# Performance work log

Measured on AMD Instinct MI355X. Metric: run time of the kernel, lower is better.

The kernel has to match this reference:

```python
import jax, jax.numpy as jnp
import numpy as np

B, T, R, A = 4, 40, 2000, 36864
H = W = 64
C = 256
PP = 7
RED = 16.0
NCLS = 21
NPOS = 64   # rois_per_image*B//4
NNEG = 192  # rois_per_image*B*3//4
DH = 1024

def _iou(b1, b2):
    # boxes are (top,left,bottom,right)
    t = jnp.maximum(b1[..., 0], b2[..., 0])
    l = jnp.maximum(b1[..., 1], b2[..., 1])
    b = jnp.minimum(b1[..., 2], b2[..., 2])
    r = jnp.minimum(b1[..., 3], b2[..., 3])
    inter = jnp.clip(b - t, 0.0) * jnp.clip(r - l, 0.0)
    a1 = (b1[..., 2] - b1[..., 0]) * (b1[..., 3] - b1[..., 1])
    a2 = (b2[..., 2] - b2[..., 0]) * (b2[..., 3] - b2[..., 1])
    return inter / (a1 + a2 - inter)

def _smooth_l1(p, t):
    d = jnp.abs(p - t)
    return jnp.mean(jnp.where(d < 1.0, 0.5 * d * d, d - 0.5))

def _roi_pool(fm, rois):
    # fm [B,C,H,W], rois [N,5] = (img_id, top,left,bottom,right) in feature-map coords
    fmt = jnp.transpose(fm, (0, 2, 3, 1))  # [B,H,W,C]
    n = rois[:, 0].astype(jnp.int32)[:, None, None]
    t, l, b, r = rois[:, 1], rois[:, 2], rois[:, 3], rois[:, 4]
    g = (jnp.arange(PP, dtype=fm.dtype) + 0.5) / PP
    ys = jnp.clip(t[:, None] + g * (b - t)[:, None], 0.0, H - 1.0)
    xs = jnp.clip(l[:, None] + g * (r - l)[:, None], 0.0, W - 1.0)
    y0 = jnp.floor(ys).astype(jnp.int32)
    x0 = jnp.floor(xs).astype(jnp.int32)
    y1 = jnp.minimum(y0 + 1, H - 1)
    x1 = jnp.minimum(x0 + 1, W - 1)
    wy = (ys - y0)[:, :, None, None]
    wx = (xs - x0)[:, None, :, None]
    def gat(yi, xi):
        return fmt[n, yi[:, :, None], xi[:, None, :], :]  # [N,PP,PP,C]
    v = (gat(y0, x0) * (1 - wy) * (1 - wx) + gat(y0, x1) * (1 - wy) * wx
         + gat(y1, x0) * wy * (1 - wx) + gat(y1, x1) * wy * wx)
    return v.reshape(v.shape[0], -1)  # [N, PP*PP*C]

def _forward(nms_reg, nms_cls, feature_maps, bboxes, classes, anchors, rpn_reg, rpn_cls, W1, b1, Wr, br, Wc, bc):
    # ---------------- RPN trainer: anchor/target matching ----------------
    iou_a = _iou(bboxes[:, :, None, :], anchors[None, None, :, :])   # [B,T,A]
    max_iou = jnp.max(iou_a, axis=1)                                  # [B,A]
    tidx = jnp.argmax(iou_a, axis=1)
    max_tgt = jnp.take_along_axis(bboxes, jnp.broadcast_to(tidx[:, :, None], (B, A, 4)), axis=1)
    mask = (max_iou > 0.5).reshape(-1)
    pos = jnp.nonzero(mask, size=128)[0]        # first 128 positives, flat order (matches cls[mask][:128])
    neg = jnp.nonzero(~mask, size=256 - B)[0]   # torch quirk: 256 - len(mask_matched) = 256 - B
    clsf = rpn_cls.reshape(-1)
    logits = jnp.concatenate([clsf[pos], clsf[neg]])
    lbl = jnp.concatenate([jnp.ones(128, dtype=logits.dtype), jnp.zeros(256 - B, dtype=logits.dtype)])
    rpn_cls_loss = jnp.mean(jnp.maximum(logits, 0) - logits * lbl + jnp.log1p(jnp.exp(-jnp.abs(logits))))
    anc_f = jnp.broadcast_to(anchors[None], (B, A, 4)).reshape(-1, 4)
    rpn_reg_loss = _smooth_l1(rpn_reg.reshape(-1, 4)[pos], max_tgt.reshape(-1, 4)[pos] - anc_f[pos]) / 4.0

    # ------------- RCNN trainer: proposal matching + sampling -------------
    iou_r = _iou(nms_reg[:, None, :, :], bboxes[:, :, None, :])  # [B,T,R]
    iou_m = jnp.max(iou_r, axis=1)                               # [B,R]
    ridx = jnp.argmax(iou_r, axis=1)
    iou_f = iou_m.reshape(-1)
    posr = jnp.nonzero(iou_f > 0.5, size=NPOS)[0]                # first NPOS positives, flat order
    negscore = jnp.where(iou_f <= 0.5, iou_f, -jnp.inf)
    negr = jax.lax.top_k(negscore, NNEG)[1]                      # negatives sorted by IoU descending
    cls_g = jnp.take_along_axis(classes, ridx, axis=1).reshape(-1)
    cls_s = jnp.concatenate([cls_g[posr], jnp.zeros(NNEG, dtype=cls_g.dtype)])
    imid = jnp.repeat(jnp.arange(B, dtype=nms_reg.dtype), R)
    nmsf = nms_reg.reshape(-1, 4)
    sel = jnp.concatenate([posr, negr])
    rois = jnp.concatenate([imid[sel][:, None], nmsf[sel]], axis=1)  # [256,5]
    feat = _roi_pool(feature_maps, rois)
    hmid = jax.nn.relu(feat @ W1 + b1)
    rreg = hmid @ Wr + br
    rcls = hmid @ Wc + bc
    logp = jax.nn.log_softmax(rcls, axis=-1)
    rcnn_cls_loss = -jnp.mean(jnp.take_along_axis(logp, cls_s[:, None], axis=1))
    posb = nmsf[posr]
    rounded = jnp.concatenate([jnp.floor(posb[:, :2] * RED), jnp.ceil(posb[:, 2:] * RED)], axis=1) / RED
    mb = jnp.take_along_axis(bboxes, jnp.broadcast_to(ridx[:, :, None], (B, R, 4)), axis=1).reshape(-1, 4)[posr]
    tgt = mb - rounded
    pr = rreg[:NPOS]
    rcnn_reg_loss = sum(_smooth_l1(pr[:, c], tgt[:, c]) for c in range(4)) / 4.0
    offset = sum(jnp.mean(jnp.abs(pr[:, c] - tgt[:, c])) for c in range(4)) / 4.0
    acc = jnp.mean((jnp.argmax(rcls[:NPOS], axis=-1) == cls_s[:NPOS]).astype(jnp.float32))
    return rpn_cls_loss, rpn_reg_loss, rcnn_cls_loss, rcnn_reg_loss, acc, offset

def _boxes(k, shape):
    k1, k2 = jax.random.split(k)
    c = jax.random.uniform(k1, shape + (2,), minval=10.0, maxval=54.0)
    h = jax.random.uniform(k2, shape + (2,), minval=3.0, maxval=8.0)
    return jnp.concatenate([c - h, c + h], axis=-1)  # (top,left,bottom,right)

def setup_inputs():
    key = jax.random.key(0)
    ks = jax.random.split(key, 13)
    base = _boxes(ks[0], (T,))
    shift = jax.random.uniform(ks[1], (B, T, 2), minval=-0.2, maxval=0.2)
    bboxes = base[None] + jnp.concatenate([shift, shift], axis=-1)  # guarantees >=128 RPN positives
    classes = jax.random.randint(ks[2], (B, T), 1, NCLS)
    anchors = _boxes(ks[3], (A,)).at[:T].set(base)
    nms_reg = _boxes(ks[4], (B, R))
    shift2 = jax.random.uniform(ks[5], (B, T, 2), minval=-0.1, maxval=0.1)
    nms_reg = nms_reg.at[:, :T].set(bboxes + jnp.concatenate([shift2, shift2], axis=-1))  # >=64 RCNN positives
    nms_cls = jax.random.normal(ks[6], (B, R))
    feature_maps = jax.random.normal(ks[7], (B, C, H, W))
    rpn_reg = 0.1 * jax.random.normal(ks[8], (B, A, 4))
    rpn_cls = jax.random.normal(ks[9], (B, A))
    D = PP * PP * C
    W1 = jax.random.normal(ks[10], (D, DH)) * float(1.0 / np.sqrt(D))
    b1 = jnp.zeros((DH,))
    Wr = jax.random.normal(ks[11], (DH, 4)) * float(1.0 / np.sqrt(DH))
    br = jnp.zeros((4,))
    Wc = jax.random.normal(ks[12], (DH, NCLS)) * float(1.0 / np.sqrt(DH))
    bc = jnp.zeros((NCLS,))
    return dict(nms_reg=nms_reg, nms_cls=nms_cls, feature_maps=feature_maps, bboxes=bboxes,
                classes=classes, anchors=anchors, rpn_reg=rpn_reg, rpn_cls=rpn_cls,
                W1=W1, b1=b1, Wr=Wr, br=br, Wc=Wc, bc=bc)

def reference(nms_reg, nms_cls, feature_maps, bboxes, classes, anchors, rpn_reg, rpn_cls, W1, b1, Wr, br, Wc, bc):
    return _forward(nms_reg, nms_cls, feature_maps, bboxes, classes, anchors, rpn_reg, rpn_cls, W1, b1, Wr, br, Wc, bc)
```

## Files before the change

### kernel.cpp

```cpp
#include <hip/hip_runtime.h>

typedef unsigned short u16;
typedef unsigned long long u64;

constexpr int cB = 4, cT = 40, cR = 2000, cA = 36864;
constexpr int cH = 64, cW = 64, cC = 256, cPP = 7;
constexpr int cNCLS = 21, cNPOS = 64, cNNEG = 192, cDH = 1024;
constexpr int cD = cPP * cPP * cC;
constexpr int cBA = cB * cA;
constexpr int cBR = cB * cR;
constexpr int NW64 = cBA / 64;
constexpr int SPLITS = 14;
constexpr int KCH = cD / SPLITS;
constexpr int BK = 64;
constexpr int NITER = KCH / BK;
constexpr unsigned POSKEY = 0x007FFFFFu;

constexpr size_t O_TIDX  = 0;
constexpr size_t O_MASKW = 589824;
constexpr size_t O_KEYS  = 608256;
constexpr size_t O_RIDXG = 640256;
constexpr size_t O_SEL   = 672256;
constexpr size_t O_CLS   = 673280;
constexpr size_t O_ROIS  = 674304;
constexpr size_t O_TGT   = 678400;
constexpr size_t O_FMT   = 1048576;
constexpr size_t O_FEAT  = O_FMT + 8388608;
constexpr size_t O_CPART = O_FEAT + 6422528;

__device__ __forceinline__ float b2f(u16 u) {
  return __uint_as_float(((unsigned)u) << 16);
}
__device__ __forceinline__ u16 f2b(float f) {
  unsigned x = __float_as_uint(f);
  unsigned r = x + 0x7FFFu + ((x >> 16) & 1u);
  return (u16)(r >> 16);
}
__device__ __forceinline__ unsigned f2key(float f) {
  unsigned b = __float_as_uint(f);
  return b ^ ((b & 0x80000000u) ? 0xFFFFFFFFu : 0x80000000u);
}

typedef __attribute__((ext_vector_type(8))) short short8;
typedef __attribute__((ext_vector_type(4))) float f32x4;

__global__ __launch_bounds__(256) void k_front(
    const float* __restrict__ bboxes, const float* __restrict__ anchors,
    const float* __restrict__ nms_reg, const float* __restrict__ fm,
    int* __restrict__ tidx, u64* __restrict__ maskw,
    unsigned* __restrict__ keys, int* __restrict__ ridxg,
    u16* __restrict__ fmt) {
  __shared__ float sfm[64 * 65];
  int bid = blockIdx.x;
  if (bid < 576) {
    float* sb = sfm;
    int b = bid / 144;
    if (threadIdx.x < cT * 4) sb[threadIdx.x] = bboxes[b * cT * 4 + threadIdx.x];
    __syncthreads();
    int i = bid * 256 + threadIdx.x;
    int a = i - b * cA;
    float4 av = ((const float4*)anchors)[a];
    float at = av.x, al = av.y, ab = av.z, ar = av.w;
    float area_a = (ab - at) * (ar - al);
    float best = -1.0f; int bi = 0;
    for (int t = 0; t < cT; ++t) {
      float bt = sb[t * 4], bl = sb[t * 4 + 1], bbv = sb[t * 4 + 2], brv = sb[t * 4 + 3];
      float ih = fmaxf(fminf(bbv, ab) - fmaxf(bt, at), 0.0f);
      float iw = fmaxf(fminf(brv, ar) - fmaxf(bl, al), 0.0f);
      float inter = ih * iw;
      float a1 = (bbv - bt) * (brv - bl);
      float iou = inter / (a1 + area_a - inter);
      if (iou > best) { best = iou; bi = t; }
    }
    tidx[i] = bi;
    u64 bal = __ballot(best > 0.5f);
    if ((threadIdx.x & 63) == 0) maskw[i >> 6] = bal;
  } else if (bid < 608) {
    float* sb = sfm;
    for (int j = threadIdx.x; j < cB * cT * 4; j += 256) sb[j] = bboxes[j];
    __syncthreads();
    int i = (bid - 576) * 256 + threadIdx.x;
    if (i >= cBR) return;
    int b = i / cR;
    float4 nv = ((const float4*)nms_reg)[i];
    float nt = nv.x, nl = nv.y, nb = nv.z, nr = nv.w;
    float area_n = (nb - nt) * (nr - nl);
    float best = -1.0f; int bi = 0;
    for (int t = 0; t < cT; ++t) {
      const float* bx = &sb[(b * cT + t) * 4];
      float ih = fmaxf(fminf(bx[2], nb) - fmaxf(bx[0], nt), 0.0f);
      float iw = fmaxf(fminf(bx[3], nr) - fmaxf(bx[1], nl), 0.0f);
      float inter = ih * iw;
      float a1 = (bx[2] - bx[0]) * (bx[3] - bx[1]);
      float iou = inter / (a1 + area_n - inter);
      if (iou > best) { best = iou; bi = t; }
    }
    keys[i] = (best <= 0.5f) ? f2key(best) : POSKEY;
    ridxg[i] = bi;
  } else {
    int f = bid - 608;
    int b = f >> 8;
    int c0 = ((f >> 6) & 3) * 64;
    int p0 = (f & 63) * 64;
    int t = threadIdx.x;
    int pL = (t & 15) * 4, cL = t >> 4;
    #pragma unroll
    for (int i = 0; i < 4; ++i) {
      int c = cL + i * 16;
      float4 v = *(const float4*)&fm[((size_t)b * cC + c0 + c) * (cH * cW) + p0 + pL];
      sfm[c * 65 + pL] = v.x; sfm[c * 65 + pL + 1] = v.y;
      sfm[c * 65 + pL + 2] = v.z; sfm[c * 65 + pL + 3] = v.w;
    }
    __syncthreads();
    int pW = t >> 2, cg = (t & 3) * 16;
    unsigned pk[8];
    #pragma unroll
    for (int j = 0; j < 8; ++j) {
      unsigned lo = f2b(sfm[(cg + 2 * j) * 65 + pW]);
      unsigned hi = f2b(sfm[(cg + 2 * j + 1) * 65 + pW]);
      pk[j] = lo | (hi << 16);
    }
    u16* dst = &fmt[((size_t)b * (cH * cW) + p0 + pW) * cC + c0 + cg];
    *(uint4*)dst = *(uint4*)&pk[0];
    *(uint4*)(dst + 8) = *(uint4*)&pk[4];
  }
}

__global__ __launch_bounds__(1024) void k_select(
    const u64* __restrict__ maskw, const int* __restrict__ tidx,
    const float* __restrict__ rpn_cls, const float* __restrict__ rpn_reg,
    const float* __restrict__ bboxes, const float* __restrict__ anchors,
    const unsigned* __restrict__ keysg, const int* __restrict__ ridxg,
    const float* __restrict__ nms_reg, const int* __restrict__ classes,
    int* __restrict__ sel, int* __restrict__ cls_s,
    float* __restrict__ rois, float* __restrict__ tgt,
    float* __restrict__ out) {
  __shared__ __align__(16) char smem[50688];
  __shared__ float s_scalF[2];
  __shared__ int s_scalI[3];
  int tid = threadIdx.x, lane = tid & 63, w = tid >> 6;
  u64 lmask = (1ULL << lane) - 1ULL;

  if (blockIdx.x == 0) {
    if (tid < 4) out[2 + tid] = 0.0f;
    u64* s_w   = (u64*)smem;
    int* s_pre = (int*)(smem + 18432);
    int* s_cw  = (int*)(smem + 19008);
    int* s_pos = (int*)(smem + 19584);
    int* s_neg = (int*)(smem + 20096);
    for (int k = tid; k < NW64; k += 1024) s_w[k] = maskw[k];
    if (tid < 128) s_pos[tid] = 0;
    if (tid < 252) s_neg[tid] = 0;
    if (tid == 0) { s_scalF[0] = 0.0f; s_scalF[1] = 0.0f; }
    __syncthreads();
    if (tid < 144) {
      int c = 0;
      #pragma unroll
      for (int k2 = 0; k2 < 16; ++k2) c += __popcll(s_w[tid * 16 + k2]);
      s_cw[tid] = c;
    }
    __syncthreads();
    if (tid == 0) {
      int run = 0;
      for (int ch = 0; ch < 144; ++ch) { s_pre[ch] = run; run += s_cw[ch]; }
    }
    __syncthreads();
    for (int ch = w; ch < 144; ch += 16) {
      int pbase = s_pre[ch];
      int nbase = ch * 1024 - pbase;
      if (pbase >= 128 && nbase >= 252) continue;
      int pc = 0;
      #pragma unroll
      for (int s2 = 0; s2 < 16; ++s2) {
        u64 word = s_w[ch * 16 + s2];
        bool m = (word >> lane) & 1ULL;
        int prefP = __popcll(word & lmask);
        int idx = ch * 1024 + s2 * 64 + lane;
        if (m) {
          int g = pbase + pc + prefP;
          if (g < 128) s_pos[g] = idx;
        } else {
          int g = nbase + (s2 * 64 + lane) - (pc + prefP);
          if (g < 252) s_neg[g] = idx;
        }
        pc += __popcll(word);
      }
    }
    __syncthreads();
    if (tid < 380) {
      int flat; float lbl;
      if (tid < 128) { flat = s_pos[tid]; lbl = 1.0f; }
      else           { flat = s_neg[tid - 128]; lbl = 0.0f; }
      float l = rpn_cls[flat];
      float term = fmaxf(l, 0.0f) - l * lbl + log1pf(expf(-fabsf(l)));
      atomicAdd(&s_scalF[0], term);
    }
    if (tid < 512) {
      int j = tid >> 2, c = tid & 3;
      int flat = s_pos[j];
      int b = flat / cA, a = flat - b * cA;
      int t = tidx[flat];
      float p = rpn_reg[flat * 4 + c];
      float tg = bboxes[(b * cT + t) * 4 + c] - anchors[a * 4 + c];
      float d = fabsf(p - tg);
      float sl = (d < 1.0f) ? 0.5f * d * d : d - 0.5f;
      atomicAdd(&s_scalF[1], sl);
    }
    __syncthreads();
    if (tid == 0) {
      out[0] = s_scalF[0] / 380.0f;
      out[1] = s_scalF[1] / 512.0f / 4.0f;
    }
  } else {
    unsigned* s_key = (unsigned*)smem;
    int* s_hist = (int*)(smem + 32000);
    int* s_pc   = (int*)(smem + 48384);
    int* s_wsum = (int*)(smem + 48896);
    int* s_wsuf = (int*)(smem + 48960);
    int* s_posr = (int*)(smem + 49024);
    int* s_negr = (int*)(smem + 49280);

    for (int i = tid; i < cBR; i += 1024) s_key[i] = keysg[i];
    if (tid < 64) s_posr[tid] = 0;
    __syncthreads();

    {
      int myv = 0; int mypre[8];
      #pragma unroll
      for (int p = 0; p < 8; ++p) {
        int i = p * 1024 + tid;
        bool v = (i < cBR) && (s_key[i] == POSKEY);
        u64 bal = __ballot(v);
        if (lane == 0) s_pc[p * 16 + w] = __popcll(bal);
        mypre[p] = __popcll(bal & lmask);
        myv |= v ? (1 << p) : 0;
      }
      __syncthreads();
      if (tid == 0) {
        int run = 0;
        for (int k = 0; k < 128; ++k) { int t = s_pc[k]; s_pc[k] = run; run += t; }
      }
      __syncthreads();
      #pragma unroll
      for (int p = 0; p < 8; ++p) {
        if (myv & (1 << p)) {
          int g = s_pc[p * 16 + w] + mypre[p];
          if (g < 64) s_posr[g] = p * 1024 + tid;
        }
      }
    }

    unsigned thr = 0; int G = 0;
    int need = cNNEG;
    #pragma unroll
    for (int lvl = 0; lvl < 3; ++lvl) {
      __syncthreads();
      #pragma unroll
      for (int k = 0; k < 4; ++k) s_hist[tid * 4 + k] = 0;
      __syncthreads();
      #pragma unroll
      for (int p = 0; p < 8; ++p) {
        int i = p * 1024 + tid;
        if (i < cBR) {
          unsigned key = s_key[i];
          int bkt = -1;
          if (lvl == 0) bkt = key >> 20;
          else if (lvl == 1) { if ((key >> 20) == (thr >> 20)) bkt = (key >> 8) & 0xFFF; }
          else { if ((key >> 8) == (thr >> 8)) bkt = (key & 0xFF) << 4; }
          if (bkt >= 0) atomicAdd(&s_hist[bkt], 1);
        }
      }
      __syncthreads();
      int local0 = s_hist[tid * 4 + 0], local1 = s_hist[tid * 4 + 1];
      int local2 = s_hist[tid * 4 + 2], local3 = s_hist[tid * 4 + 3];
      int lsum = local0 + local1 + local2 + local3;
      int x = lsum;
      #pragma unroll
      for (int off = 1; off < 64; off <<= 1) {
        int t = __shfl_down(x, off, 64);
        if (lane + off < 64) x += t;
      }
      if (lane == 0) s_wsum[w] = x;
      __syncthreads();
      if (tid == 0) {
        int run = 0;
        for (int wi = 15; wi >= 0; --wi) { s_wsuf[wi] = run; run += s_wsum[wi]; }
      }
      __syncthreads();
      int above = s_wsuf[w] + (x - lsum);
      int run = above;
      int loc[4] = {local3, local2, local1, local0};
      #pragma unroll
      for (int j = 0; j < 4; ++j) {
        int S = run + loc[j];
        if (run < need && S >= need) { s_scalI[0] = tid * 4 + (3 - j); s_scalI[1] = run; }
        run = S;
      }
      __syncthreads();
      int bS = s_scalI[0], ov = s_scalI[1];
      if (lvl == 0) thr = ((unsigned)bS) << 20;
      else if (lvl == 1) thr |= ((unsigned)bS) << 8;
      else thr |= ((unsigned)bS) >> 4;
      G += ov;
      need -= ov;
    }

    if (tid == 0) s_scalI[2] = 0;
    __syncthreads();
    #pragma unroll
    for (int p = 0; p < 8; ++p) {
      int i = p * 1024 + tid;
      if (i < cBR && s_key[i] > thr) {
        int slot = atomicAdd(&s_scalI[2], 1);
        s_negr[slot] = i;
      }
    }
    {
      __syncthreads();
      int myv = 0; int mypre[8];
      #pragma unroll
      for (int p = 0; p < 8; ++p) {
        int i = p * 1024 + tid;
        bool v = (i < cBR) && (s_key[i] == thr);
        u64 bal = __ballot(v);
        if (lane == 0) s_pc[p * 16 + w] = __popcll(bal);
        mypre[p] = __popcll(bal & lmask);
        myv |= v ? (1 << p) : 0;
      }
      __syncthreads();
      if (tid == 0) {
        int run = 0;
        for (int k = 0; k < 128; ++k) { int t = s_pc[k]; s_pc[k] = run; run += t; }
      }
      __syncthreads();
      #pragma unroll
      for (int p = 0; p < 8; ++p) {
        if (myv & (1 << p)) {
          int g = s_pc[p * 16 + w] + mypre[p];
          if (g < need) s_negr[G + g] = p * 1024 + tid;
        }
      }
    }
    __syncthreads();

    if (tid < 256) {
      int flat = (tid < 64) ? s_posr[tid] : s_negr[tid - 64];
      sel[tid] = flat;
      int b = flat / cR;
      #pragma unroll
      for (int c = 0; c < 4; ++c) rois[tid * 4 + c] = nms_reg[flat * 4 + c];
      cls_s[tid] = (tid < 64) ? classes[b * cT + ridxg[flat]] : 0;
      if (tid < 64) {
        int mt = ridxg[flat];
        #pragma unroll
        for (int c = 0; c < 4; ++c) {
          float v = nms_reg[flat * 4 + c];
          float rr = ((c < 2) ? floorf(v * 16.0f) : ceilf(v * 16.0f)) / 16.0f;
          float mbv = bboxes[(b * cT + mt) * 4 + c];
          tgt[tid * 4 + c] = mbv - rr;
        }
      }
    }
  }
}

__global__ void k_roi_pool(const u16* __restrict__ fmt, const float* __restrict__ rois,
                           const int* __restrict__ sel, u16* __restrict__ feat) {
  int j = blockIdx.x;
  int py = blockIdx.y;
  int c = threadIdx.x;
  int flat = sel[j];
  int n = flat / cR;
  float t = rois[j * 4 + 0], l = rois[j * 4 + 1];
  float bb = rois[j * 4 + 2], r = rois[j * 4 + 3];
  const u16* base = fmt + (size_t)n * (cH * cW) * cC;
  float gy = (py + 0.5f) / (float)cPP;
  float ys = fminf(fmaxf(t + gy * (bb - t), 0.0f), 63.0f);
  int y0 = (int)floorf(ys);
  int y1 = min(y0 + 1, 63);
  float wy = ys - (float)y0;
  #pragma unroll
  for (int px = 0; px < cPP; ++px) {
    float gx = (px + 0.5f) / (float)cPP;
    float xs = fminf(fmaxf(l + gx * (r - l), 0.0f), 63.0f);
    int x0 = (int)floorf(xs);
    int x1 = min(x0 + 1, 63);
    float wx = xs - (float)x0;
    float f00 = b2f(base[(y0 * cW + x0) * cC + c]);
    float f01 = b2f(base[(y0 * cW + x1) * cC + c]);
    float f10 = b2f(base[(y1 * cW + x0) * cC + c]);
    float f11 = b2f(base[(y1 * cW + x1) * cC + c]);
    float v = f00 * (1.0f - wy) * (1.0f - wx) + f01 * (1.0f - wy) * wx +
              f10 * wy * (1.0f - wx) + f11 * wy * wx;
    feat[((size_t)j * 49 + py * cPP + px) * cC + c] = f2b(v);
  }
}

__global__ __launch_bounds__(256) void k_gemm1(const u16* __restrict__ feat, const float* __restrict__ W1,
                                               float* __restrict__ Cpart) {
  __shared__ u16 Bs[2][32][64];
  int tid = threadIdx.x;
  int bid = blockIdx.x;
  int ksp = bid >> 5;
  int n0 = (bid & 31) * 32;
  int kb0 = ksp * KCH;
  int lane = tid & 63, w = tid >> 6;
  int r = lane & 15, q = lane >> 4;
  int rb = r & 7;

  f32x4 acc[4][2] = {};

  int bn = tid & 31, kq = tid >> 5;
  int bswz = (kq ^ (bn & 7)) * 8;
  const float* bp0 = &W1[(size_t)(kb0 + kq * 8) * cDH + n0 + bn];

  int offK0 = (q ^ rb) * 8;
  int offK1 = ((4 + q) ^ rb) * 8;

  const u16* afp = &feat[(size_t)(w * 64 + r) * cD + kb0 + q * 8];

  float BR[4][8];
  short8 A[2][4][2];

#define LOADB(slot, ph) { const float* _bp = bp0 + (size_t)(ph) * BK * cDH; \
    _Pragma("unroll") \
    for (int j = 0; j < 8; ++j) BR[slot][j] = _bp[(size_t)j * cDH]; }
#define STOREB(buf, slot) { \
    union { u16 u[8]; uint4 v; } pb; \
    _Pragma("unroll") \
    for (int j = 0; j < 8; ++j) pb.u[j] = f2b(BR[slot][j]); \
    *(uint4*)&Bs[buf][bn][bswz] = pb.v; }
#define LOADA(set, ph) { const u16* _p = afp + (ph) * 64; \
    _Pragma("unroll") \
    for (int mf = 0; mf < 4; ++mf) { \
      A[set][mf][0] = *(const short8*)(_p + (size_t)mf * 16 * cD); \
      A[set][mf][1] = *(const short8*)(_p + (size_t)mf * 16 * cD + 32); \
    } }
#define COMPUTE(buf, set) { \
    short8 b00 = *(const short8*)&Bs[buf][r][offK0]; \
    short8 b10 = *(const short8*)&Bs[buf][16 + r][offK0]; \
    short8 b01 = *(const short8*)&Bs[buf][r][offK1]; \
    short8 b11 = *(const short8*)&Bs[buf][16 + r][offK1]; \
    _Pragma("unroll") \
    for (int mf = 0; mf < 4; ++mf) { \
      acc[mf][0] = __builtin_amdgcn_mfma_f32_16x16x32_bf16(A[set][mf][0], b00, acc[mf][0], 0, 0, 0); \
      acc[mf][1] = __builtin_amdgcn_mfma_f32_16x16x32_bf16(A[set][mf][0], b10, acc[mf][1], 0, 0, 0); \
      acc[mf][0] = __builtin_amdgcn_mfma_f32_16x16x32_bf16(A[set][mf][1], b01, acc[mf][0], 0, 0, 0); \
      acc[mf][1] = __builtin_amdgcn_mfma_f32_16x16x32_bf16(A[set][mf][1], b11, acc[mf][1], 0, 0, 0); \
    } }
#define BARRIER() { \
    asm volatile("s_waitcnt lgkmcnt(0)" ::: "memory"); \
    __builtin_amdgcn_s_barrier(); \
    __builtin_amdgcn_sched_barrier(0); }

  LOADB(0, 0); LOADB(1, 1); LOADB(2, 2); LOADB(3, 3);
  LOADA(0, 0); LOADA(1, 1);
  STOREB(0, 0);
  BARRIER();

  #pragma unroll
  for (int p = 0; p < NITER; ++p) {
    if (p + 1 < NITER) STOREB((p + 1) & 1, (p + 1) & 3);
    if (p + 4 < NITER) LOADB(p & 3, p + 4);
    __builtin_amdgcn_s_setprio(1);
    COMPUTE(p & 1, p & 1);
    __builtin_amdgcn_s_setprio(0);
    if (p + 2 < NITER) LOADA(p & 1, p + 2);
    BARRIER();
  }

#undef LOADB
#undef STOREB
#undef LOADA
#undef COMPUTE
#undef BARRIER

  float* Cp = Cpart + (size_t)ksp * 256 * cDH;
  #pragma unroll
  for (int mf = 0; mf < 4; ++mf) {
    #pragma unroll
    for (int rg = 0; rg < 4; ++rg) {
      int row = w * 64 + mf * 16 + q * 4 + rg;
      Cp[(size_t)row * cDH + n0 + r] = acc[mf][0][rg];
      Cp[(size_t)row * cDH + n0 + 16 + r] = acc[mf][1][rg];
    }
  }
}

__global__ __launch_bounds__(256) void k_heads(
    const float* __restrict__ Cpart, const float* __restrict__ b1,
    const float* __restrict__ Wr, const float* __restrict__ br,
    const float* __restrict__ Wc, const float* __restrict__ bc,
    const int* __restrict__ cls_s, const float* __restrict__ tgt,
    float* __restrict__ out) {
  __shared__ float sacc[25];
  int row = blockIdx.x, tid = threadIdx.x, lane = tid & 63;
  if (tid < 25) sacc[tid] = 0.0f;
  __syncthreads();
  int k0 = tid * 4;
  float4 h = *(const float4*)&b1[k0];
  #pragma unroll
  for (int s = 0; s < SPLITS; ++s) {
    float4 c = *(const float4*)&Cpart[(size_t)s * 256 * cDH + (size_t)row * cDH + k0];
    h.x += c.x; h.y += c.y; h.z += c.z; h.w += c.w;
  }
  float hv[4] = {fmaxf(h.x, 0.f), fmaxf(h.y, 0.f), fmaxf(h.z, 0.f), fmaxf(h.w, 0.f)};
  float part[25];
  #pragma unroll
  for (int c = 0; c < 25; ++c) part[c] = 0.0f;
  #pragma unroll
  for (int j = 0; j < 4; ++j) {
    float4 wr = *(const float4*)&Wr[(k0 + j) * 4];
    part[0] += hv[j] * wr.x; part[1] += hv[j] * wr.y;
    part[2] += hv[j] * wr.z; part[3] += hv[j] * wr.w;
    const float* wc = &Wc[(k0 + j) * 21];
    #pragma unroll
    for (int c = 0; c < 21; ++c) part[4 + c] += hv[j] * wc[c];
  }
  #pragma unroll
  for (int off = 32; off; off >>= 1) {
    #pragma unroll
    for (int c = 0; c < 25; ++c) part[c] += __shfl_down(part[c], off, 64);
  }
  if (lane == 0) {
    #pragma unroll
    for (int c = 0; c < 25; ++c) atomicAdd(&sacc[c], part[c]);
  }
  __syncthreads();
  if (tid == 0) {
    int cls = cls_s[row];
    float m = -INFINITY;
    float vals[21];
    #pragma unroll
    for (int c = 0; c < 21; ++c) { vals[c] = sacc[4 + c] + bc[c]; m = fmaxf(m, vals[c]); }
    float sum = 0.0f;
    #pragma unroll
    for (int c = 0; c < 21; ++c) sum += expf(vals[c] - m);
    float lse = m + logf(sum);
    atomicAdd(&out[2], (lse - vals[cls]) * (1.0f / 256.0f));
    if (row < 64) {
      int am2 = 0; float bv = vals[0];
      #pragma unroll
      for (int c = 1; c < 21; ++c) if (vals[c] > bv) { bv = vals[c]; am2 = c; }
      if (am2 == cls) atomicAdd(&out[4], 1.0f / 64.0f);
    }
  }
  if (tid == 1 && row < 64) {
    float sl = 0.0f, of = 0.0f;
    #pragma unroll
    for (int c = 0; c < 4; ++c) {
      float d = fabsf((sacc[c] + br[c]) - tgt[row * 4 + c]);
      sl += (d < 1.0f) ? 0.5f * d * d : d - 0.5f;
      of += d;
    }
    atomicAdd(&out[3], sl * (1.0f / 256.0f));
    atomicAdd(&out[5], of * (1.0f / 256.0f));
  }
}

extern "C" void kernel_launch(void* const* d_in, const int* in_sizes, int n_in,
                              void* d_out, int out_size, void* d_ws, size_t ws_size,
                              hipStream_t stream) {
  const float* nms_reg = (const float*)d_in[0];
  const float* fm      = (const float*)d_in[2];
  const float* bboxes  = (const float*)d_in[3];
  const int*   classes = (const int*)d_in[4];
  const float* anchors = (const float*)d_in[5];
  const float* rpn_reg = (const float*)d_in[6];
  const float* rpn_cls = (const float*)d_in[7];
  const float* W1      = (const float*)d_in[8];
  const float* b1      = (const float*)d_in[9];
  const float* Wr      = (const float*)d_in[10];
  const float* br      = (const float*)d_in[11];
  const float* Wc      = (const float*)d_in[12];
  const float* bc      = (const float*)d_in[13];
  float* out = (float*)d_out;
  char* ws = (char*)d_ws;

  int*      tidx  = (int*)(ws + O_TIDX);
  u64*      maskw = (u64*)(ws + O_MASKW);
  unsigned* keys  = (unsigned*)(ws + O_KEYS);
  int*      ridxg = (int*)(ws + O_RIDXG);
  int*      sel   = (int*)(ws + O_SEL);
  int*      clss  = (int*)(ws + O_CLS);
  float*    rois  = (float*)(ws + O_ROIS);
  float*    tgt   = (float*)(ws + O_TGT);
  u16*      fmt   = (u16*)(ws + O_FMT);
  u16*      feat  = (u16*)(ws + O_FEAT);
  float*    Cpart = (float*)(ws + O_CPART);

  k_front<<<608 + 1024, 256, 0, stream>>>(bboxes, anchors, nms_reg, fm,
                                          tidx, maskw, keys, ridxg, fmt);
  k_select<<<2, 1024, 0, stream>>>(maskw, tidx, rpn_cls, rpn_reg, bboxes, anchors,
                                   keys, ridxg, nms_reg, classes, sel, clss, rois, tgt, out);
  k_roi_pool<<<dim3(256, cPP), 256, 0, stream>>>(fmt, rois, sel, feat);
  k_gemm1<<<448, 256, 0, stream>>>(feat, W1, Cpart);
  k_heads<<<256, 256, 0, stream>>>(Cpart, b1, Wr, br, Wc, bc, clss, tgt, out);
}
```

Measured before the change: 189.9 us.

## Pre-transpose W1 to bf16 in front kernel and split GEMM over M tiles

W1 is now converted to bf16 and transposed to [N,K] inside the front kernel, using 3136 extra blocks that run alongside the other front-stage work. The GEMM then loads B with contiguous 16-byte vector reads instead of strided fp32 loads converted per tile. The GEMM is also split into 4 M-tiles of 64 rows, giving 1792 blocks with one 16-row fragment per wave, and block ids are remapped so neighbouring blocks spread across XCDs. The cost is an extra 8 MB bf16 weight write and read, plus each B tile being fetched by four blocks instead of one.

```diff
diff --git a/kernel.cpp b/kernel.cpp
--- a/kernel.cpp
+++ b/kernel.cpp
@@ -27,6 +27,7 @@
 constexpr size_t O_FMT   = 1048576;
 constexpr size_t O_FEAT  = O_FMT + 8388608;
 constexpr size_t O_CPART = O_FEAT + 6422528;
+constexpr size_t O_WT    = O_CPART + 14680064;
 
 __device__ __forceinline__ float b2f(u16 u) {
   return __uint_as_float(((unsigned)u) << 16);
@@ -47,9 +48,10 @@
 __global__ __launch_bounds__(256) void k_front(
     const float* __restrict__ bboxes, const float* __restrict__ anchors,
     const float* __restrict__ nms_reg, const float* __restrict__ fm,
+    const float* __restrict__ W1,
     int* __restrict__ tidx, u64* __restrict__ maskw,
     unsigned* __restrict__ keys, int* __restrict__ ridxg,
-    u16* __restrict__ fmt) {
+    u16* __restrict__ fmt, u16* __restrict__ wt) {
   __shared__ float sfm[64 * 65];
   int bid = blockIdx.x;
   if (bid < 576) {
@@ -97,7 +99,7 @@
     }
     keys[i] = (best <= 0.5f) ? f2key(best) : POSKEY;
     ridxg[i] = bi;
-  } else {
+  } else if (bid < 1632) {
     int f = bid - 608;
     int b = f >> 8;
     int c0 = ((f >> 6) & 3) * 64;
@@ -121,6 +123,31 @@
       pk[j] = lo | (hi << 16);
     }
     u16* dst = &fmt[((size_t)b * (cH * cW) + p0 + pW) * cC + c0 + cg];
+    *(uint4*)dst = *(uint4*)&pk[0];
+    *(uint4*)(dst + 8) = *(uint4*)&pk[4];
+  } else {
+    int f = bid - 1632;
+    int kt = f % 196, nt = f / 196;
+    int k0 = kt * 64, n0 = nt * 64;
+    int t = threadIdx.x;
+    int n4 = (t & 15) * 4, kL = t >> 4;
+    #pragma unroll
+    for (int i = 0; i < 4; ++i) {
+      int k = kL + i * 16;
+      float4 v = *(const float4*)&W1[(size_t)(k0 + k) * cDH + n0 + n4];
+      sfm[k * 65 + n4] = v.x; sfm[k * 65 + n4 + 1] = v.y;
+      sfm[k * 65 + n4 + 2] = v.z; sfm[k * 65 + n4 + 3] = v.w;
+    }
+    __syncthreads();
+    int n = t >> 2, kc = (t & 3) * 16;
+    unsigned pk[8];
+    #pragma unroll
+    for (int j = 0; j < 8; ++j) {
+      unsigned lo = f2b(sfm[(kc + 2 * j) * 65 + n]);
+      unsigned hi = f2b(sfm[(kc + 2 * j + 1) * 65 + n]);
+      pk[j] = lo | (hi << 16);
+    }
+    u16* dst = &wt[(size_t)(n0 + n) * cD + k0 + kc];
     *(uint4*)dst = *(uint4*)&pk[0];
     *(uint4*)(dst + 8) = *(uint4*)&pk[4];
   }
@@ -396,58 +423,50 @@
   }
 }
 
-__global__ __launch_bounds__(256) void k_gemm1(const u16* __restrict__ feat, const float* __restrict__ W1,
+__global__ __launch_bounds__(256) void k_gemm1(const u16* __restrict__ feat, const u16* __restrict__ Wt,
                                                float* __restrict__ Cpart) {
   __shared__ u16 Bs[2][32][64];
   int tid = threadIdx.x;
   int bid = blockIdx.x;
-  int ksp = bid >> 5;
-  int n0 = (bid & 31) * 32;
+  int xcd = bid & 7, jj = bid >> 3;
+  int gl = jj >> 2, m = jj & 3;
+  int g = gl * 8 + xcd;
+  int n0 = (g & 31) * 32;
+  int ksp = g >> 5;
   int kb0 = ksp * KCH;
+  int m0 = m * 64;
   int lane = tid & 63, w = tid >> 6;
   int r = lane & 15, q = lane >> 4;
   int rb = r & 7;
 
-  f32x4 acc[4][2] = {};
-
-  int bn = tid & 31, kq = tid >> 5;
-  int bswz = (kq ^ (bn & 7)) * 8;
-  const float* bp0 = &W1[(size_t)(kb0 + kq * 8) * cDH + n0 + bn];
+  f32x4 acc0 = {}, acc1 = {};
+
+  int bn = tid >> 3, bc = tid & 7;
+  int bcs = (bc ^ (bn & 7)) * 8;
+  const u16* bp0 = &Wt[(size_t)(n0 + bn) * cD + kb0 + bc * 8];
 
   int offK0 = (q ^ rb) * 8;
   int offK1 = ((4 + q) ^ rb) * 8;
 
-  const u16* afp = &feat[(size_t)(w * 64 + r) * cD + kb0 + q * 8];
-
-  float BR[4][8];
-  short8 A[2][4][2];
-
-#define LOADB(slot, ph) { const float* _bp = bp0 + (size_t)(ph) * BK * cDH; \
-    _Pragma("unroll") \
-    for (int j = 0; j < 8; ++j) BR[slot][j] = _bp[(size_t)j * cDH]; }
-#define STOREB(buf, slot) { \
-    union { u16 u[8]; uint4 v; } pb; \
-    _Pragma("unroll") \
-    for (int j = 0; j < 8; ++j) pb.u[j] = f2b(BR[slot][j]); \
-    *(uint4*)&Bs[buf][bn][bswz] = pb.v; }
-#define LOADA(set, ph) { const u16* _p = afp + (ph) * 64; \
-    _Pragma("unroll") \
-    for (int mf = 0; mf < 4; ++mf) { \
-      A[set][mf][0] = *(const short8*)(_p + (size_t)mf * 16 * cD); \
-      A[set][mf][1] = *(const short8*)(_p + (size_t)mf * 16 * cD + 32); \
-    } }
+  const u16* afp = &feat[(size_t)(m0 + w * 16 + r) * cD + kb0 + q * 8];
+
+  uint4 BR[4];
+  short8 A[2][2];
+
+#define LOADB(slot, ph) { BR[slot] = *(const uint4*)(bp0 + (ph) * BK); }
+#define STOREB(buf, slot) { *(uint4*)&Bs[buf][bn][bcs] = BR[slot]; }
+#define LOADA(set, ph) { const u16* _p = afp + (ph) * BK; \
+    A[set][0] = *(const short8*)_p; \
+    A[set][1] = *(const short8*)(_p + 32); }
 #define COMPUTE(buf, set) { \
     short8 b00 = *(const short8*)&Bs[buf][r][offK0]; \
     short8 b10 = *(const short8*)&Bs[buf][16 + r][offK0]; \
     short8 b01 = *(const short8*)&Bs[buf][r][offK1]; \
     short8 b11 = *(const short8*)&Bs[buf][16 + r][offK1]; \
-    _Pragma("unroll") \
-    for (int mf = 0; mf < 4; ++mf) { \
-      acc[mf][0] = __builtin_amdgcn_mfma_f32_16x16x32_bf16(A[set][mf][0], b00, acc[mf][0], 0, 0, 0); \
-      acc[mf][1] = __builtin_amdgcn_mfma_f32_16x16x32_bf16(A[set][mf][0], b10, acc[mf][1], 0, 0, 0); \
-      acc[mf][0] = __builtin_amdgcn_mfma_f32_16x16x32_bf16(A[set][mf][1], b01, acc[mf][0], 0, 0, 0); \
-      acc[mf][1] = __builtin_amdgcn_mfma_f32_16x16x32_bf16(A[set][mf][1], b11, acc[mf][1], 0, 0, 0); \
-    } }
+    acc0 = __builtin_amdgcn_mfma_f32_16x16x32_bf16(A[set][0], b00, acc0, 0, 0, 0); \
+    acc1 = __builtin_amdgcn_mfma_f32_16x16x32_bf16(A[set][0], b10, acc1, 0, 0, 0); \
+    acc0 = __builtin_amdgcn_mfma_f32_16x16x32_bf16(A[set][1], b01, acc0, 0, 0, 0); \
+    acc1 = __builtin_amdgcn_mfma_f32_16x16x32_bf16(A[set][1], b11, acc1, 0, 0, 0); }
 #define BARRIER() { \
     asm volatile("s_waitcnt lgkmcnt(0)" ::: "memory"); \
     __builtin_amdgcn_s_barrier(); \
@@ -477,13 +496,10 @@
 
   float* Cp = Cpart + (size_t)ksp * 256 * cDH;
   #pragma unroll
-  for (int mf = 0; mf < 4; ++mf) {
-    #pragma unroll
-    for (int rg = 0; rg < 4; ++rg) {
-      int row = w * 64 + mf * 16 + q * 4 + rg;
-      Cp[(size_t)row * cDH + n0 + r] = acc[mf][0][rg];
-      Cp[(size_t)row * cDH + n0 + 16 + r] = acc[mf][1][rg];
-    }
+  for (int rg = 0; rg < 4; ++rg) {
+    int row = m0 + w * 16 + q * 4 + rg;
+    Cp[(size_t)row * cDH + n0 + r] = acc0[rg];
+    Cp[(size_t)row * cDH + n0 + 16 + r] = acc1[rg];
   }
 }
 
@@ -588,12 +604,13 @@
   u16*      fmt   = (u16*)(ws + O_FMT);
   u16*      feat  = (u16*)(ws + O_FEAT);
   float*    Cpart = (float*)(ws + O_CPART);
-
-  k_front<<<608 + 1024, 256, 0, stream>>>(bboxes, anchors, nms_reg, fm,
-                                          tidx, maskw, keys, ridxg, fmt);
+  u16*      wt    = (u16*)(ws + O_WT);
+
+  k_front<<<608 + 1024 + 3136, 256, 0, stream>>>(bboxes, anchors, nms_reg, fm, W1,
+                                                 tidx, maskw, keys, ridxg, fmt, wt);
   k_select<<<2, 1024, 0, stream>>>(maskw, tidx, rpn_cls, rpn_reg, bboxes, anchors,
                                    keys, ridxg, nms_reg, classes, sel, clss, rois, tgt, out);
   k_roi_pool<<<dim3(256, cPP), 256, 0, stream>>>(fmt, rois, sel, feat);
-  k_gemm1<<<448, 256, 0, stream>>>(feat, W1, Cpart);
+  k_gemm1<<<1792, 256, 0, stream>>>(feat, wt, Cpart);
   k_heads<<<256, 256, 0, stream>>>(Cpart, b1, Wr, br, Wc, bc, clss, tgt, out);
 }
```

New measurement: 192.3 us. About the same (+1.3%).
